# Optimization experiments

Hardware: AMD Instinct MI355X
Metric: run time of the kernel (lower is better)

## Reference

```python
import jax, jax.numpy as jnp
import numpy as np

N_NODES = 50000
N_EDGES = 800000
IN_DIM = 128
HID = 128
BN_EPS = 1e-5


def _linear_init(key, fan_in, fan_out):
    kw, kb = jax.random.split(key)
    bound = 1.0 / np.sqrt(fan_in)
    w = jax.random.uniform(kw, (fan_in, fan_out), minval=-bound, maxval=bound, dtype=jnp.float32)
    b = jax.random.uniform(kb, (fan_out,), minval=-bound, maxval=bound, dtype=jnp.float32)
    return w, b


def setup_inputs() -> dict:
    key = jax.random.key(0)
    ks = jax.random.split(key, 8)
    x = jax.random.normal(ks[0], (N_NODES, IN_DIM), dtype=jnp.float32)
    edge_index = jax.random.randint(ks[1], (2, N_EDGES), 0, N_NODES, dtype=jnp.int32)
    # GIN layer 0 MLP: Linear(IN_DIM,HID) -> ReLU -> Linear(HID,HID)
    w0a, b0a = _linear_init(ks[2], IN_DIM, HID)
    w0b, b0b = _linear_init(ks[3], HID, HID)
    # GIN layer 1 MLP
    w1a, b1a = _linear_init(ks[4], HID, HID)
    w1b, b1b = _linear_init(ks[5], HID, HID)
    # encoder BatchNorm affine params (torch init: gamma=1, beta=0)
    bn_gamma = jnp.ones((HID,), jnp.float32)
    bn_beta = jnp.zeros((HID,), jnp.float32)
    # projection head: Linear(HID,HID) -> BatchNorm -> PReLU -> Dropout
    pw, pb = _linear_init(ks[6], HID, HID)
    pbn_gamma = jnp.ones((HID,), jnp.float32)
    pbn_beta = jnp.zeros((HID,), jnp.float32)
    prelu_a = jnp.asarray(0.25, jnp.float32)  # torch PReLU default init
    return {
        'x': x, 'edge_index': edge_index,
        'w0a': w0a, 'b0a': b0a, 'w0b': w0b, 'b0b': b0b,
        'w1a': w1a, 'b1a': b1a, 'w1b': w1b, 'b1b': b1b,
        'bn_gamma': bn_gamma, 'bn_beta': bn_beta,
        'pw': pw, 'pb': pb, 'pbn_gamma': pbn_gamma, 'pbn_beta': pbn_beta,
        'prelu_a': prelu_a,
    }


def _batch_norm(x, gamma, beta):
    # training-mode BatchNorm1d: biased variance over the node (batch) dim
    mu = jnp.mean(x, axis=0)
    var = jnp.var(x, axis=0)
    return gamma * (x - mu) * jax.lax.rsqrt(var + BN_EPS) + beta


def _gin_conv(z, src, dst, wa, ba, wb, bb):
    # sum-aggregate neighbor features: out[i] = (1+eps)*z[i] + sum_{j->i} z[j], eps=0
    agg = jax.ops.segment_sum(z[src], dst, num_segments=N_NODES)
    h = z + agg
    h = jax.nn.relu(h @ wa + ba)
    return h @ wb + bb


def reference(x, edge_index, w0a, b0a, w0b, b0b, w1a, b1a, w1b, b1b,
              bn_gamma, bn_beta, pw, pb, pbn_gamma, pbn_beta, prelu_a):
    src, dst = edge_index[0], edge_index[1]
    z = x
    z = jax.nn.relu(_gin_conv(z, src, dst, w0a, b0a, w0b, b0b))  # dropout: identity (deterministic)
    z = jax.nn.relu(_gin_conv(z, src, dst, w1a, b1a, w1b, b1b))
    z = _batch_norm(z, bn_gamma, bn_beta)
    p = z @ pw + pb
    p = _batch_norm(p, pbn_gamma, pbn_beta)
    p = jnp.where(p > 0, p, prelu_a * p)  # PReLU, single shared parameter
    return z, p
```

## Files before the change

### kernel.cpp

```cpp
#include <hip/hip_runtime.h>
#include <hip/hip_bf16.h>

#define NN 50000
#define NE 800000
#define HD 128
#define BN_EPS 1e-5f
#define MSTR 132
#define NBUK 782
#define PB 200
#define CHUNK 4000

typedef __attribute__((ext_vector_type(8))) __bf16 bf16x8;
typedef __attribute__((ext_vector_type(4))) __bf16 bf16x4;
typedef __attribute__((ext_vector_type(4))) float floatx4;

__global__ __launch_bounds__(256) void k_prep(const float* __restrict__ W0,
                                              const float* __restrict__ W1,
                                              const float* __restrict__ W2,
                                              const float* __restrict__ W3,
                                              const float* __restrict__ W4,
                                              __bf16* __restrict__ Bh,
                                              __bf16* __restrict__ Bl,
                                              const float* __restrict__ X,
                                              __bf16* __restrict__ Y,
                                              const int* __restrict__ dst,
                                              int* __restrict__ gbtot) {
    __shared__ int h[NBUK];
    const int b = blockIdx.x;
    if (b < 320) {
        const int t = b * 256 + threadIdx.x;
        const int m = t >> 14;
        const int rem = t & 16383;
        const int n = rem >> 7;
        const int k = rem & 127;
        const float* W = (m == 0) ? W0 : (m == 1) ? W1 : (m == 2) ? W2 : (m == 3) ? W3 : W4;
        const float w = W[k * HD + n];
        const __bf16 hi = (__bf16)w;
        const int ct = n >> 4, lm = n & 15;
        const int ks = k >> 5, lq = (k & 31) >> 3, j = k & 7;
        const int lane = lq * 16 + lm;
        const size_t o = (size_t)m * HD * HD + (size_t)(((ct * 4 + ks) * 64) + lane) * 8 + j;
        Bh[o] = hi;
        Bl[o] = (__bf16)(w - (float)hi);
    } else if (b < 320 + 3125) {
        const int i8 = ((b - 320) * 256 + threadIdx.x) * 8;
        const float4 a = *(const float4*)&X[i8];
        const float4 c = *(const float4*)&X[i8 + 4];
        bf16x8 o;
        o[0] = (__bf16)a.x; o[1] = (__bf16)a.y; o[2] = (__bf16)a.z; o[3] = (__bf16)a.w;
        o[4] = (__bf16)c.x; o[5] = (__bf16)c.y; o[6] = (__bf16)c.z; o[7] = (__bf16)c.w;
        *(bf16x8*)&Y[i8] = o;
    } else {
        for (int i = threadIdx.x; i < NBUK; i += 256) h[i] = 0;
        __syncthreads();
        const int e0 = (b - (320 + 3125)) * CHUNK;
        for (int i = threadIdx.x; i < CHUNK; i += 256)
            atomicAdd(&h[dst[e0 + i] >> 6], 1);
        __syncthreads();
        for (int i = threadIdx.x; i < NBUK; i += 256) {
            const int v = h[i];
            if (v) atomicAdd(&gbtot[i], v);
        }
    }
}

__global__ __launch_bounds__(256) void k_bscan(const int* __restrict__ gbtot,
                                               int* __restrict__ bbase,
                                               int* __restrict__ gcur,
                                               int* __restrict__ rowptr) {
    __shared__ int sh[256];
    const int t = threadIdx.x;
    int v[4];
    int s = 0;
#pragma unroll
    for (int j = 0; j < 4; ++j) {
        const int idx = t * 4 + j;
        v[j] = (idx < NBUK) ? gbtot[idx] : 0;
        s += v[j];
    }
    sh[t] = s;
    __syncthreads();
#pragma unroll
    for (int st = 1; st < 256; st <<= 1) {
        int add = (t >= st) ? sh[t - st] : 0;
        __syncthreads();
        sh[t] += add;
        __syncthreads();
    }
    int run = sh[t] - s;
#pragma unroll
    for (int j = 0; j < 4; ++j) {
        const int idx = t * 4 + j;
        if (idx < NBUK) { bbase[idx] = run; gcur[idx] = run; }
        run += v[j];
    }
    if (t == 255) bbase[NBUK] = run;
    if (t == 0) rowptr[NN] = NE;
}

__global__ __launch_bounds__(256) void k_bscatter(const int* __restrict__ src,
                                                  const int* __restrict__ dst,
                                                  int* __restrict__ gcur,
                                                  int2* __restrict__ pairs) {
    __shared__ int h[NBUK];
    __shared__ int cur[NBUK];
    for (int i = threadIdx.x; i < NBUK; i += 256) h[i] = 0;
    __syncthreads();
    const int e0 = blockIdx.x * CHUNK;
    for (int i = threadIdx.x; i < CHUNK; i += 256)
        atomicAdd(&h[dst[e0 + i] >> 6], 1);
    __syncthreads();
    for (int i = threadIdx.x; i < NBUK; i += 256) {
        const int v = h[i];
        if (v) cur[i] = atomicAdd(&gcur[i], v);
    }
    __syncthreads();
    for (int i = threadIdx.x; i < CHUNK; i += 256) {
        const int d = dst[e0 + i];
        const int pos = atomicAdd(&cur[d >> 6], 1);
        pairs[pos] = make_int2(src[e0 + i], d);
    }
}

__global__ __launch_bounds__(256) void k_csrfin(const int2* __restrict__ pairs,
                                                const int* __restrict__ bbase,
                                                int* __restrict__ rowptr,
                                                int* __restrict__ esrc) {
    __shared__ int cnt[64], lof[64], cur[64];
    const int b = blockIdx.x;
    const int s = bbase[b], e = bbase[b + 1];
    const int tid = threadIdx.x;
    if (tid < 64) cnt[tid] = 0;
    __syncthreads();
    for (int i = s + tid; i < e; i += 256)
        atomicAdd(&cnt[pairs[i].y & 63], 1);
    __syncthreads();
    if (tid == 0) {
        int r = 0;
#pragma unroll
        for (int j = 0; j < 64; ++j) { lof[j] = r; cur[j] = r; r += cnt[j]; }
    }
    __syncthreads();
    if (tid < 64) {
        const int node = b * 64 + tid;
        if (node < NN) rowptr[node] = s + lof[tid];
    }
    for (int i = s + tid; i < e; i += 256) {
        const int2 p = pairs[i];
        const int pos = atomicAdd(&cur[p.y & 63], 1);
        esrc[s + pos] = p.x;
    }
}

__device__ __forceinline__ void split8(const float4 a, const float4 b,
                                       bf16x8& hi, bf16x8& lo) {
    hi[0] = (__bf16)a.x; lo[0] = (__bf16)(a.x - (float)hi[0]);
    hi[1] = (__bf16)a.y; lo[1] = (__bf16)(a.y - (float)hi[1]);
    hi[2] = (__bf16)a.z; lo[2] = (__bf16)(a.z - (float)hi[2]);
    hi[3] = (__bf16)a.w; lo[3] = (__bf16)(a.w - (float)hi[3]);
    hi[4] = (__bf16)b.x; lo[4] = (__bf16)(b.x - (float)hi[4]);
    hi[5] = (__bf16)b.y; lo[5] = (__bf16)(b.y - (float)hi[5]);
    hi[6] = (__bf16)b.z; lo[6] = (__bf16)(b.z - (float)hi[6]);
    hi[7] = (__bf16)b.w; lo[7] = (__bf16)(b.w - (float)hi[7]);
}

__device__ __forceinline__ void addb8(float4& a, float4& b, const bf16x8 v) {
    a.x += (float)v[0]; a.y += (float)v[1]; a.z += (float)v[2]; a.w += (float)v[3];
    b.x += (float)v[4]; b.y += (float)v[5]; b.z += (float)v[6]; b.w += (float)v[7];
}

__global__ __launch_bounds__(256) void k_aggb(const __bf16* __restrict__ Z,
                                              const int* __restrict__ rowptr,
                                              const int* __restrict__ esrc,
                                              float* __restrict__ H) {
    const int g = threadIdx.x >> 4;
    const int lg = threadIdx.x & 15;
    const int node = blockIdx.x * 16 + g;
    const int cb = lg * 8;
    const int start = rowptr[node], end = rowptr[node + 1];
    float4 a = {0.f, 0.f, 0.f, 0.f}, b = {0.f, 0.f, 0.f, 0.f};
    addb8(a, b, *(const bf16x8*)&Z[(size_t)node * HD + cb]);
    int k = start;
    for (; k + 8 <= end; k += 8) {
        const int s0 = esrc[k + 0], s1 = esrc[k + 1];
        const int s2 = esrc[k + 2], s3 = esrc[k + 3];
        const int s4 = esrc[k + 4], s5 = esrc[k + 5];
        const int s6 = esrc[k + 6], s7 = esrc[k + 7];
        const bf16x8 v0 = *(const bf16x8*)&Z[(size_t)s0 * HD + cb];
        const bf16x8 v1 = *(const bf16x8*)&Z[(size_t)s1 * HD + cb];
        const bf16x8 v2 = *(const bf16x8*)&Z[(size_t)s2 * HD + cb];
        const bf16x8 v3 = *(const bf16x8*)&Z[(size_t)s3 * HD + cb];
        const bf16x8 v4 = *(const bf16x8*)&Z[(size_t)s4 * HD + cb];
        const bf16x8 v5 = *(const bf16x8*)&Z[(size_t)s5 * HD + cb];
        const bf16x8 v6 = *(const bf16x8*)&Z[(size_t)s6 * HD + cb];
        const bf16x8 v7 = *(const bf16x8*)&Z[(size_t)s7 * HD + cb];
        addb8(a, b, v0); addb8(a, b, v1); addb8(a, b, v2); addb8(a, b, v3);
        addb8(a, b, v4); addb8(a, b, v5); addb8(a, b, v6); addb8(a, b, v7);
    }
    for (; k + 4 <= end; k += 4) {
        const int s0 = esrc[k + 0], s1 = esrc[k + 1];
        const int s2 = esrc[k + 2], s3 = esrc[k + 3];
        const bf16x8 v0 = *(const bf16x8*)&Z[(size_t)s0 * HD + cb];
        const bf16x8 v1 = *(const bf16x8*)&Z[(size_t)s1 * HD + cb];
        const bf16x8 v2 = *(const bf16x8*)&Z[(size_t)s2 * HD + cb];
        const bf16x8 v3 = *(const bf16x8*)&Z[(size_t)s3 * HD + cb];
        addb8(a, b, v0); addb8(a, b, v1); addb8(a, b, v2); addb8(a, b, v3);
    }
    for (; k < end; ++k) {
        const int s = esrc[k];
        addb8(a, b, *(const bf16x8*)&Z[(size_t)s * HD + cb]);
    }
    *(float4*)&H[(size_t)node * HD + cb] = a;
    *(float4*)&H[(size_t)node * HD + cb + 4] = b;
}

struct StageRegs { bf16x8 v[4]; };

__device__ __forceinline__ void stage_load(StageRegs& s, const __bf16* __restrict__ Bh,
                                           const __bf16* __restrict__ Bl,
                                           int ks, int wid, int lane) {
#pragma unroll
    for (int i = 0; i < 4; ++i) {
        const int chunk = wid * 4 + i;
        const int ct = chunk & 7;
        const __bf16* base = (chunk < 8) ? Bh : Bl;
        s.v[i] = *(const bf16x8*)&base[(size_t)(((ct * 4 + ks) * 64) + lane) * 8];
    }
}
__device__ __forceinline__ void stage_write(const StageRegs& s, __bf16* Bb,
                                            int wid, int lane) {
#pragma unroll
    for (int i = 0; i < 4; ++i) {
        const int chunk = wid * 4 + i;
        *(bf16x8*)&Bb[chunk * 512 + lane * 8] = s.v[i];
    }
}

__device__ __forceinline__ void mfma_pass_lds(floatx4 (&acc)[8], const bf16x8 ah,
                                              const bf16x8 al, const __bf16* Bb,
                                              int lane) {
    bf16x8 bh[8], bl[8];
#pragma unroll
    for (int ct = 0; ct < 8; ++ct) {
        bh[ct] = *(const bf16x8*)&Bb[ct * 512 + lane * 8];
        bl[ct] = *(const bf16x8*)&Bb[(8 + ct) * 512 + lane * 8];
    }
    __builtin_amdgcn_sched_barrier(0);
#pragma unroll
    for (int ct = 0; ct < 8; ++ct) {
        acc[ct] = __builtin_amdgcn_mfma_f32_16x16x32_bf16(al, bh[ct], acc[ct], 0, 0, 0);
        acc[ct] = __builtin_amdgcn_mfma_f32_16x16x32_bf16(ah, bl[ct], acc[ct], 0, 0, 0);
        acc[ct] = __builtin_amdgcn_mfma_f32_16x16x32_bf16(ah, bh[ct], acc[ct], 0, 0, 0);
    }
}

template <int STATS, int OUT16>
__global__ __launch_bounds__(256) void k_mlp(const float* __restrict__ A,
                                             const __bf16* __restrict__ Bh1,
                                             const __bf16* __restrict__ Bl1,
                                             const float* __restrict__ b1,
                                             const __bf16* __restrict__ Bh2,
                                             const __bf16* __restrict__ Bl2,
                                             const float* __restrict__ b2,
                                             float* __restrict__ C,
                                             __bf16* __restrict__ C16,
                                             float* __restrict__ pstat) {
    __shared__ float mid[4][16 * MSTR];
    __shared__ __bf16 Bb[2][16 * 512];
    __shared__ float ssum[128], ssq[128];
    const int tid = threadIdx.x;
    const int wid = tid >> 6, lane = tid & 63;
    const int lq = lane >> 4, lm = lane & 15;
    if (STATS && tid < 128) { ssum[tid] = 0.f; ssq[tid] = 0.f; }
    const int rowbase = blockIdx.x * 64 + wid * 16;
    const int r0 = min(rowbase + lm, NN - 1);
    float* m = &mid[wid][0];

    bf16x8 ahv[4], alv[4];
    {
        float4 av[8];
#pragma unroll
        for (int ks = 0; ks < 4; ++ks) {
            const int kk = ks * 32 + lq * 8;
            av[ks * 2 + 0] = *(const float4*)&A[(size_t)r0 * HD + kk];
            av[ks * 2 + 1] = *(const float4*)&A[(size_t)r0 * HD + kk + 4];
        }
#pragma unroll
        for (int ks = 0; ks < 4; ++ks)
            split8(av[ks * 2], av[ks * 2 + 1], ahv[ks], alv[ks]);
    }
    {
        StageRegs s;
        stage_load(s, Bh1, Bl1, 0, wid, lane);
        stage_write(s, &Bb[0][0], wid, lane);
    }
    __syncthreads();

    floatx4 acc[8];
#pragma unroll
    for (int j = 0; j < 8; ++j) acc[j] = (floatx4){0.f, 0.f, 0.f, 0.f};

#pragma unroll
    for (int p = 0; p < 8; ++p) {
        StageRegs s;
        if (p < 7) {
            const int pn = p + 1;
            stage_load(s, (pn < 4) ? Bh1 : Bh2, (pn < 4) ? Bl1 : Bl2, pn & 3, wid, lane);
        }
        bf16x8 ah, al;
        if (p < 4) { ah = ahv[p]; al = alv[p]; }
        else {
            const int kk = (p & 3) * 32 + lq * 8;
            const float4 aa = *(const float4*)&m[lm * MSTR + kk];
            const float4 ab = *(const float4*)&m[lm * MSTR + kk + 4];
            split8(aa, ab, ah, al);
        }
        mfma_pass_lds(acc, ah, al, &Bb[p & 1][0], lane);
        if (p == 3) {
#pragma unroll
            for (int ct = 0; ct < 8; ++ct) {
                const int col = ct * 16 + lm;
                const float bcol = b1[col];
#pragma unroll
                for (int r = 0; r < 4; ++r)
                    m[(lq * 4 + r) * MSTR + col] = fmaxf(acc[ct][r] + bcol, 0.f);
            }
#pragma unroll
            for (int j = 0; j < 8; ++j) acc[j] = (floatx4){0.f, 0.f, 0.f, 0.f};
        }
        if (p < 7) stage_write(s, &Bb[(p + 1) & 1][0], wid, lane);
        __syncthreads();
    }
#pragma unroll
    for (int ct = 0; ct < 8; ++ct) {
        const int col = ct * 16 + lm;
        const float bcol = b2[col];
#pragma unroll
        for (int r = 0; r < 4; ++r)
            m[(lq * 4 + r) * MSTR + col] = fmaxf(acc[ct][r] + bcol, 0.f);
    }
    float s0 = 0.f, s1 = 0.f, s2 = 0.f, s3 = 0.f;
    float q0 = 0.f, q1 = 0.f, q2 = 0.f, q3 = 0.f;
    const int c0 = (lane * 4) & 127;
#pragma unroll
    for (int p = 0; p < 8; ++p) {
        const int idx = p * 256 + lane * 4;
        const int r = idx >> 7;
        const float4 v = *(const float4*)&m[r * MSTR + c0];
        const int row = rowbase + r;
        if (row < NN) {
            if (OUT16) {
                bf16x4 o;
                o[0] = (__bf16)v.x; o[1] = (__bf16)v.y;
                o[2] = (__bf16)v.z; o[3] = (__bf16)v.w;
                *(bf16x4*)&C16[(size_t)row * HD + c0] = o;
            } else {
                *(float4*)&C[(size_t)row * HD + c0] = v;
            }
            if (STATS) {
                s0 += v.x; q0 = fmaf(v.x, v.x, q0);
                s1 += v.y; q1 = fmaf(v.y, v.y, q1);
                s2 += v.z; q2 = fmaf(v.z, v.z, q2);
                s3 += v.w; q3 = fmaf(v.w, v.w, q3);
            }
        }
    }
    if (STATS) {
        s0 += __shfl_xor(s0, 32); q0 += __shfl_xor(q0, 32);
        s1 += __shfl_xor(s1, 32); q1 += __shfl_xor(q1, 32);
        s2 += __shfl_xor(s2, 32); q2 += __shfl_xor(q2, 32);
        s3 += __shfl_xor(s3, 32); q3 += __shfl_xor(q3, 32);
        if (lane < 32) {
            atomicAdd(&ssum[c0 + 0], s0); atomicAdd(&ssq[c0 + 0], q0);
            atomicAdd(&ssum[c0 + 1], s1); atomicAdd(&ssq[c0 + 1], q1);
            atomicAdd(&ssum[c0 + 2], s2); atomicAdd(&ssq[c0 + 2], q2);
            atomicAdd(&ssum[c0 + 3], s3); atomicAdd(&ssq[c0 + 3], q3);
        }
        __syncthreads();
        if (tid < 128) {
            pstat[(size_t)blockIdx.x * 256 + tid] = ssum[tid];
            pstat[(size_t)blockIdx.x * 256 + 128 + tid] = ssq[tid];
        }
    }
}

__global__ __launch_bounds__(256) void k_proj(const float* __restrict__ Z2,
                                              const float* __restrict__ bnsc,
                                              const float* __restrict__ bnsh,
                                              float* __restrict__ Zout,
                                              const __bf16* __restrict__ Bh,
                                              const __bf16* __restrict__ Bl,
                                              const float* __restrict__ bias,
                                              float* __restrict__ C,
                                              float* __restrict__ pstat) {
    __shared__ union {
        __bf16 bb[2][16 * 512];
        float tb[4][16 * MSTR];
    } u;
    __shared__ float ssum[128], ssq[128];
    const int tid = threadIdx.x;
    const int wid = tid >> 6, lane = tid & 63;
    const int lq = lane >> 4, lm = lane & 15;
    if (tid < 128) { ssum[tid] = 0.f; ssq[tid] = 0.f; }
    const int rowbase = blockIdx.x * 64 + wid * 16;
    const int r0 = min(rowbase + lm, NN - 1);
    const bool rowok = (rowbase + lm) < NN;
    float* m = &u.tb[wid][0];

    bf16x8 ahv[4], alv[4];
#pragma unroll
    for (int ks = 0; ks < 4; ++ks) {
        const int kk = ks * 32 + lq * 8;
        const float4 za = *(const float4*)&Z2[(size_t)r0 * HD + kk];
        const float4 zb = *(const float4*)&Z2[(size_t)r0 * HD + kk + 4];
        const float4 sca = *(const float4*)&bnsc[kk];
        const float4 scb = *(const float4*)&bnsc[kk + 4];
        const float4 sha = *(const float4*)&bnsh[kk];
        const float4 shb = *(const float4*)&bnsh[kk + 4];
        float4 aa, ab;
        aa.x = fmaf(za.x, sca.x, sha.x); aa.y = fmaf(za.y, sca.y, sha.y);
        aa.z = fmaf(za.z, sca.z, sha.z); aa.w = fmaf(za.w, sca.w, sha.w);
        ab.x = fmaf(zb.x, scb.x, shb.x); ab.y = fmaf(zb.y, scb.y, shb.y);
        ab.z = fmaf(zb.z, scb.z, shb.z); ab.w = fmaf(zb.w, scb.w, shb.w);
        if (rowok) {
            *(float4*)&Zout[(size_t)r0 * HD + kk] = aa;
            *(float4*)&Zout[(size_t)r0 * HD + kk + 4] = ab;
        }
        split8(aa, ab, ahv[ks], alv[ks]);
    }
    {
        StageRegs s;
        stage_load(s, Bh, Bl, 0, wid, lane);
        stage_write(s, &u.bb[0][0], wid, lane);
    }
    __syncthreads();

    floatx4 acc[8];
#pragma unroll
    for (int j = 0; j < 8; ++j) acc[j] = (floatx4){0.f, 0.f, 0.f, 0.f};
#pragma unroll
    for (int p = 0; p < 4; ++p) {
        StageRegs s;
        if (p < 3) stage_load(s, Bh, Bl, p + 1, wid, lane);
        mfma_pass_lds(acc, ahv[p], alv[p], &u.bb[p & 1][0], lane);
        if (p < 3) stage_write(s, &u.bb[(p + 1) & 1][0], wid, lane);
        __syncthreads();
    }
#pragma unroll
    for (int ct = 0; ct < 8; ++ct) {
        const int col = ct * 16 + lm;
        const float bcol = bias[col];
#pragma unroll
        for (int r = 0; r < 4; ++r)
            m[(lq * 4 + r) * MSTR + col] = acc[ct][r] + bcol;
    }
    float s0 = 0.f, s1 = 0.f, s2 = 0.f, s3 = 0.f;
    float q0 = 0.f, q1 = 0.f, q2 = 0.f, q3 = 0.f;
    const int c0 = (lane * 4) & 127;
#pragma unroll
    for (int p = 0; p < 8; ++p) {
        const int idx = p * 256 + lane * 4;
        const int r = idx >> 7;
        const float4 v = *(const float4*)&m[r * MSTR + c0];
        const int row = rowbase + r;
        if (row < NN) {
            *(float4*)&C[(size_t)row * HD + c0] = v;
            s0 += v.x; q0 = fmaf(v.x, v.x, q0);
            s1 += v.y; q1 = fmaf(v.y, v.y, q1);
            s2 += v.z; q2 = fmaf(v.z, v.z, q2);
            s3 += v.w; q3 = fmaf(v.w, v.w, q3);
        }
    }
    s0 += __shfl_xor(s0, 32); q0 += __shfl_xor(q0, 32);
    s1 += __shfl_xor(s1, 32); q1 += __shfl_xor(q1, 32);
    s2 += __shfl_xor(s2, 32); q2 += __shfl_xor(q2, 32);
    s3 += __shfl_xor(s3, 32); q3 += __shfl_xor(q3, 32);
    if (lane < 32) {
        atomicAdd(&ssum[c0 + 0], s0); atomicAdd(&ssq[c0 + 0], q0);
        atomicAdd(&ssum[c0 + 1], s1); atomicAdd(&ssq[c0 + 1], q1);
        atomicAdd(&ssum[c0 + 2], s2); atomicAdd(&ssq[c0 + 2], q2);
        atomicAdd(&ssum[c0 + 3], s3); atomicAdd(&ssq[c0 + 3], q3);
    }
    __syncthreads();
    if (tid < 128) {
        pstat[(size_t)blockIdx.x * 256 + tid] = ssum[tid];
        pstat[(size_t)blockIdx.x * 256 + 128 + tid] = ssq[tid];
    }
}

__global__ __launch_bounds__(256) void k_sred(const float* __restrict__ ps, int nblk,
                                              float* __restrict__ out) {
    const int j = threadIdx.x;
    float acc = 0.f;
    for (int r = blockIdx.x; r < nblk; r += 64)
        acc += ps[(size_t)r * 256 + j];
    out[blockIdx.x * 256 + j] = acc;
}

__global__ void k_bnfin(const float* __restrict__ pb2,
                        const float* __restrict__ gamma, const float* __restrict__ beta,
                        float* __restrict__ scale, float* __restrict__ shift) {
    const int c = threadIdx.x;
    float s = 0.f, q = 0.f;
    for (int b = 0; b < 64; ++b) {
        s += pb2[b * 256 + c];
        q += pb2[b * 256 + 128 + c];
    }
    const float mean = s * (1.f / NN);
    const float var = q * (1.f / NN) - mean * mean;
    const float sc = gamma[c] * rsqrtf(var + BN_EPS);
    scale[c] = sc;
    shift[c] = beta[c] - mean * sc;
}

__global__ void k_bnapply(const float* __restrict__ X, const float* __restrict__ scale,
                          const float* __restrict__ shift, float* __restrict__ Y,
                          const float* __restrict__ pa) {
    const int i4 = (blockIdx.x * 256 + threadIdx.x) * 4;
    const int c = i4 & 127;
    const float4 sc = *(const float4*)&scale[c];
    const float4 sh = *(const float4*)&shift[c];
    const float4 v = *(const float4*)&X[i4];
    float4 y;
    y.x = fmaf(v.x, sc.x, sh.x);
    y.y = fmaf(v.y, sc.y, sh.y);
    y.z = fmaf(v.z, sc.z, sh.z);
    y.w = fmaf(v.w, sc.w, sh.w);
    const float a = pa[0];
    if (y.x < 0.f) y.x *= a;
    if (y.y < 0.f) y.y *= a;
    if (y.z < 0.f) y.z *= a;
    if (y.w < 0.f) y.w *= a;
    *(float4*)&Y[i4] = y;
}

extern "C" void kernel_launch(void* const* d_in, const int* in_sizes, int n_in,
                              void* d_out, int out_size, void* d_ws, size_t ws_size,
                              hipStream_t stream) {
    const float* x = (const float*)d_in[0];
    const int* ei = (const int*)d_in[1];
    const float* w0a = (const float*)d_in[2];
    const float* b0a = (const float*)d_in[3];
    const float* w0b = (const float*)d_in[4];
    const float* b0b = (const float*)d_in[5];
    const float* w1a = (const float*)d_in[6];
    const float* b1a = (const float*)d_in[7];
    const float* w1b = (const float*)d_in[8];
    const float* b1b = (const float*)d_in[9];
    const float* bng = (const float*)d_in[10];
    const float* bnb = (const float*)d_in[11];
    const float* pw  = (const float*)d_in[12];
    const float* pb  = (const float*)d_in[13];
    const float* pbng = (const float*)d_in[14];
    const float* pbnb = (const float*)d_in[15];
    const float* pa = (const float*)d_in[16];

    float* outZ = (float*)d_out;
    float* outP = outZ + (size_t)NN * HD;

    float* ws = (float*)d_ws;
    float* bufH = ws;
    float* st = bufH + (size_t)NN * HD;
    int* rowptr = (int*)(st + 1024);
    int* esrc = rowptr + NN + 64;
    int* gbtot = esrc + NE;
    int* bbase = gbtot + 800;
    int* gcur = bbase + 800;
    __bf16* wth = (__bf16*)(gcur + 800);
    __bf16* wtl = wth + 5 * HD * HD;
    float* ps1 = (float*)(wtl + 5 * HD * HD);
    float* pb2a = ps1 + 800 * 256;
    float* ps2 = pb2a + 64 * 256;
    float* pb2b = ps2 + 800 * 256;

    __bf16* xb  = (__bf16*)bufH;
    __bf16* z1b = xb + (size_t)NN * HD;
    int2* pairs = (int2*)z1b;
    float* Hbuf = outP;

    const int* srcv = ei;
    const int* dstv = ei + NE;

    const int ELV = (NN * HD) / (256 * 4);
    const int GB = (NN + 63) / 64;
    const int AB = NN / 16;
    const int PREPB = 320 + 3125 + PB;

    hipMemsetAsync(gbtot, 0, 800 * sizeof(int), stream);
    k_prep<<<PREPB, 256, 0, stream>>>(w0a, w0b, w1a, w1b, pw, wth, wtl,
                                      x, xb, dstv, gbtot);

    k_bscan<<<1, 256, 0, stream>>>(gbtot, bbase, gcur, rowptr);
    k_bscatter<<<PB, 256, 0, stream>>>(srcv, dstv, gcur, pairs);
    k_csrfin<<<NBUK, 256, 0, stream>>>(pairs, bbase, rowptr, esrc);

    k_aggb<<<AB, 256, 0, stream>>>(xb, rowptr, esrc, Hbuf);
    k_mlp<0, 1><<<GB, 256, 0, stream>>>(Hbuf,
                                        wth + 0 * HD * HD, wtl + 0 * HD * HD, b0a,
                                        wth + 1 * HD * HD, wtl + 1 * HD * HD, b0b,
                                        nullptr, z1b, nullptr);

    k_aggb<<<AB, 256, 0, stream>>>(z1b, rowptr, esrc, Hbuf);
    k_mlp<1, 0><<<GB, 256, 0, stream>>>(Hbuf,
                                        wth + 2 * HD * HD, wtl + 2 * HD * HD, b1a,
                                        wth + 3 * HD * HD, wtl + 3 * HD * HD, b1b,
                                        outP, nullptr, ps1);

    k_sred<<<64, 256, 0, stream>>>(ps1, GB, pb2a);
    k_bnfin<<<1, 128, 0, stream>>>(pb2a, bng, bnb, st + 256, st + 384);
    k_proj<<<GB, 256, 0, stream>>>(outP, st + 256, st + 384, outZ,
                                   wth + 4 * HD * HD, wtl + 4 * HD * HD, pb,
                                   outP, ps2);

    k_sred<<<64, 256, 0, stream>>>(ps2, GB, pb2b);
    k_bnfin<<<1, 128, 0, stream>>>(pb2b, pbng, pbnb, st + 768, st + 896);
    k_bnapply<<<ELV, 256, 0, stream>>>(outP, st + 768, st + 896, outP, pa);
}
```

Baseline: 311.5 us.

## Pack edge pairs into 32-bit words, unroll gather by 16, fuse BN finalize into projection

Edge (src, dst-low-bits) pairs are packed into a single 32-bit word instead of an int2, which halves scatter and CSR-finalize traffic. The aggregation loop issues 16 gathers at a time to expose more memory-level parallelism. The encoder BatchNorm finalize kernel is removed, and every projection block now recomputes scale and shift from the 64 partial sums, saving a launch at the cost of redundant per-block reads. The wider unroll raises register pressure, and the packing relies on node ids fitting in 17 bits.

Measured after the change: 311.1 us (median of 2 runs). Within noise of the previous version (-0.1%).

```diff
diff --git a/kernel.cpp b/kernel.cpp
--- a/kernel.cpp
+++ b/kernel.cpp
@@ -101,7 +101,7 @@
 __global__ __launch_bounds__(256) void k_bscatter(const int* __restrict__ src,
                                                   const int* __restrict__ dst,
                                                   int* __restrict__ gcur,
-                                                  int2* __restrict__ pairs) {
+                                                  unsigned* __restrict__ pairs) {
     __shared__ int h[NBUK];
     __shared__ int cur[NBUK];
     for (int i = threadIdx.x; i < NBUK; i += 256) h[i] = 0;
@@ -118,11 +118,11 @@
     for (int i = threadIdx.x; i < CHUNK; i += 256) {
         const int d = dst[e0 + i];
         const int pos = atomicAdd(&cur[d >> 6], 1);
-        pairs[pos] = make_int2(src[e0 + i], d);
-    }
-}
-
-__global__ __launch_bounds__(256) void k_csrfin(const int2* __restrict__ pairs,
+        pairs[pos] = ((unsigned)(d & 63) << 17) | (unsigned)src[e0 + i];
+    }
+}
+
+__global__ __launch_bounds__(256) void k_csrfin(const unsigned* __restrict__ pairs,
                                                 const int* __restrict__ bbase,
                                                 int* __restrict__ rowptr,
                                                 int* __restrict__ esrc) {
@@ -133,7 +133,7 @@
     if (tid < 64) cnt[tid] = 0;
     __syncthreads();
     for (int i = s + tid; i < e; i += 256)
-        atomicAdd(&cnt[pairs[i].y & 63], 1);
+        atomicAdd(&cnt[pairs[i] >> 17], 1);
     __syncthreads();
     if (tid == 0) {
         int r = 0;
@@ -146,9 +146,9 @@
         if (node < NN) rowptr[node] = s + lof[tid];
     }
     for (int i = s + tid; i < e; i += 256) {
-        const int2 p = pairs[i];
-        const int pos = atomicAdd(&cur[p.y & 63], 1);
-        esrc[s + pos] = p.x;
+        const unsigned p = pairs[i];
+        const int pos = atomicAdd(&cur[p >> 17], 1);
+        esrc[s + pos] = (int)(p & 0x1FFFFu);
     }
 }
 
@@ -181,21 +181,15 @@
     float4 a = {0.f, 0.f, 0.f, 0.f}, b = {0.f, 0.f, 0.f, 0.f};
     addb8(a, b, *(const bf16x8*)&Z[(size_t)node * HD + cb]);
     int k = start;
-    for (; k + 8 <= end; k += 8) {
-        const int s0 = esrc[k + 0], s1 = esrc[k + 1];
-        const int s2 = esrc[k + 2], s3 = esrc[k + 3];
-        const int s4 = esrc[k + 4], s5 = esrc[k + 5];
-        const int s6 = esrc[k + 6], s7 = esrc[k + 7];
-        const bf16x8 v0 = *(const bf16x8*)&Z[(size_t)s0 * HD + cb];
-        const bf16x8 v1 = *(const bf16x8*)&Z[(size_t)s1 * HD + cb];
-        const bf16x8 v2 = *(const bf16x8*)&Z[(size_t)s2 * HD + cb];
-        const bf16x8 v3 = *(const bf16x8*)&Z[(size_t)s3 * HD + cb];
-        const bf16x8 v4 = *(const bf16x8*)&Z[(size_t)s4 * HD + cb];
-        const bf16x8 v5 = *(const bf16x8*)&Z[(size_t)s5 * HD + cb];
-        const bf16x8 v6 = *(const bf16x8*)&Z[(size_t)s6 * HD + cb];
-        const bf16x8 v7 = *(const bf16x8*)&Z[(size_t)s7 * HD + cb];
-        addb8(a, b, v0); addb8(a, b, v1); addb8(a, b, v2); addb8(a, b, v3);
-        addb8(a, b, v4); addb8(a, b, v5); addb8(a, b, v6); addb8(a, b, v7);
+    for (; k + 16 <= end; k += 16) {
+        int s[16];
+#pragma unroll
+        for (int j = 0; j < 16; ++j) s[j] = esrc[k + j];
+        bf16x8 v[16];
+#pragma unroll
+        for (int j = 0; j < 16; ++j) v[j] = *(const bf16x8*)&Z[(size_t)s[j] * HD + cb];
+#pragma unroll
+        for (int j = 0; j < 16; ++j) addb8(a, b, v[j]);
     }
     for (; k + 4 <= end; k += 4) {
         const int s0 = esrc[k + 0], s1 = esrc[k + 1];
@@ -385,8 +379,9 @@
 }
 
 __global__ __launch_bounds__(256) void k_proj(const float* __restrict__ Z2,
-                                              const float* __restrict__ bnsc,
-                                              const float* __restrict__ bnsh,
+                                              const float* __restrict__ pb2a,
+                                              const float* __restrict__ gamma,
+                                              const float* __restrict__ beta,
                                               float* __restrict__ Zout,
                                               const __bf16* __restrict__ Bh,
                                               const __bf16* __restrict__ Bl,
@@ -398,10 +393,24 @@
         float tb[4][16 * MSTR];
     } u;
     __shared__ float ssum[128], ssq[128];
+    __shared__ float scs[128], shs[128];
     const int tid = threadIdx.x;
     const int wid = tid >> 6, lane = tid & 63;
     const int lq = lane >> 4, lm = lane & 15;
-    if (tid < 128) { ssum[tid] = 0.f; ssq[tid] = 0.f; }
+    if (tid < 128) {
+        ssum[tid] = 0.f; ssq[tid] = 0.f;
+        float s = 0.f, q = 0.f;
+        for (int b = 0; b < 64; ++b) {
+            s += pb2a[b * 256 + tid];
+            q += pb2a[b * 256 + 128 + tid];
+        }
+        const float mean = s * (1.f / NN);
+        const float var = q * (1.f / NN) - mean * mean;
+        const float sc = gamma[tid] * rsqrtf(var + BN_EPS);
+        scs[tid] = sc;
+        shs[tid] = beta[tid] - mean * sc;
+    }
+    __syncthreads();
     const int rowbase = blockIdx.x * 64 + wid * 16;
     const int r0 = min(rowbase + lm, NN - 1);
     const bool rowok = (rowbase + lm) < NN;
@@ -413,10 +422,10 @@
         const int kk = ks * 32 + lq * 8;
         const float4 za = *(const float4*)&Z2[(size_t)r0 * HD + kk];
         const float4 zb = *(const float4*)&Z2[(size_t)r0 * HD + kk + 4];
-        const float4 sca = *(const float4*)&bnsc[kk];
-        const float4 scb = *(const float4*)&bnsc[kk + 4];
-        const float4 sha = *(const float4*)&bnsh[kk];
-        const float4 shb = *(const float4*)&bnsh[kk + 4];
+        const float4 sca = *(const float4*)&scs[kk];
+        const float4 scb = *(const float4*)&scs[kk + 4];
+        const float4 sha = *(const float4*)&shs[kk];
+        const float4 shb = *(const float4*)&shs[kk + 4];
         float4 aa, ab;
         aa.x = fmaf(za.x, sca.x, sha.x); aa.y = fmaf(za.y, sca.y, sha.y);
         aa.z = fmaf(za.z, sca.z, sha.z); aa.w = fmaf(za.w, sca.w, sha.w);
@@ -575,7 +584,7 @@
 
     __bf16* xb  = (__bf16*)bufH;
     __bf16* z1b = xb + (size_t)NN * HD;
-    int2* pairs = (int2*)z1b;
+    unsigned* pairs = (unsigned*)z1b;
     float* Hbuf = outP;
 
     const int* srcv = ei;
@@ -607,8 +616,7 @@
                                         outP, nullptr, ps1);
 
     k_sred<<<64, 256, 0, stream>>>(ps1, GB, pb2a);
-    k_bnfin<<<1, 128, 0, stream>>>(pb2a, bng, bnb, st + 256, st + 384);
-    k_proj<<<GB, 256, 0, stream>>>(outP, st + 256, st + 384, outZ,
+    k_proj<<<GB, 256, 0, stream>>>(outP, pb2a, bng, bnb, outZ,
                                    wth + 4 * HD * HD, wtl + 4 * HD * HD, pb,
                                    outP, ps2);
 
```
